# Performance work log

Hardware: AMD Instinct MI355X
Metric: run time of the kernel (lower is better)

## Reference

```python
import jax, jax.numpy as jnp
import numpy as np

S, F, C = 256, 128, 16          # seq_len, n_files, len_feature_columns
T_HEADS, M_HEADS = 5, 4


def _pos_encoding(max_len, d):
    pos = jnp.arange(max_len, dtype=jnp.float32)[:, None]
    div = jnp.exp(jnp.arange(0, d, 2, dtype=jnp.float32) * (-np.log(10000.0) / d))
    pe = jnp.zeros((max_len, d), jnp.float32)
    pe = pe.at[:, 0::2].set(jnp.sin(pos * div))
    pe = pe.at[:, 1::2].set(jnp.cos(pos * div))
    return pe


def _ln(x, w, b, eps=1e-5):
    mu = jnp.mean(x, -1, keepdims=True)
    var = jnp.mean((x - mu) ** 2, -1, keepdims=True)
    return (x - mu) * jax.lax.rsqrt(var + eps) * w + b


def _softmax_kernel(data, proj, is_query, eps=1e-4):
    # FAVOR+ positive softmax random features (lucidrains performer default)
    dh = data.shape[-1]
    m = proj.shape[0]
    dn = dh ** -0.25
    ratio = m ** -0.5
    dd = jnp.einsum('bhnd,md->bhnm', data * dn, proj)
    diag = jnp.sum(data ** 2, -1, keepdims=True) * 0.5 * dn * dn
    stab = jnp.max(dd, -1, keepdims=True) if is_query else jnp.max(dd)
    return ratio * (jnp.exp(dd - diag - stab) + eps)


def _favor_attn(x, wq, wk, wv, wo, wo_b, proj, heads):
    b, n, _ = x.shape
    inner = wq.shape[1]
    dh = inner // heads
    split = lambda t: t.reshape(b, n, heads, dh).transpose(0, 2, 1, 3)
    q, k, v = split(x @ wq), split(x @ wk), split(x @ wv)
    qp = _softmax_kernel(q, proj, True)   # [b,h,n,m]
    kp = _softmax_kernel(k, proj, False)  # [b,h,n,m]
    d_inv = 1.0 / jnp.einsum('bhnm,bhm->bhn', qp, jnp.sum(kp, 2))
    ctx = jnp.einsum('bhnm,bhnd->bhmd', kp, v)            # O(n*m*d) linear attention
    out = jnp.einsum('bhnm,bhmd,bhn->bhnd', qp, ctx, d_inv)
    return out.transpose(0, 2, 1, 3).reshape(b, n, inner) @ wo + wo_b


def _performer(x, p, heads):
    (ln1w, ln1b, wq, wk, wv, wo, wob, ln2w, ln2b, f1w, f1b, f2w, f2b, proj) = p
    for l in range(ln1w.shape[0]):  # depth=4, structurally distinct params
        x = x + _favor_attn(_ln(x, ln1w[l], ln1b[l]), wq[l], wk[l], wv[l], wo[l], wob[l], proj[l], heads)
        h = _ln(x, ln2w[l], ln2b[l])
        x = x + (jax.nn.gelu(h @ f1w[l] + f1b[l]) @ f2w[l] + f2b[l])
    return x


def setup_inputs() -> dict:
    key = jax.random.key(0)
    keys = iter(jax.random.split(key, 80))
    nrm = lambda shape, s=0.02: jax.random.normal(next(keys), shape, jnp.float32) * s
    B = 64
    d = {"x": jax.random.normal(next(keys), (B, S, F * C), jnp.float32),
         "lin_w": nrm((F, C)), "lin_b": jnp.zeros((F,), jnp.float32)}

    def perf(prefix, D, heads, dh, M, L=4):
        I = heads * dh
        d[prefix + "ln1_w"] = jnp.ones((L, D), jnp.float32)
        d[prefix + "ln1_b"] = jnp.zeros((L, D), jnp.float32)
        d[prefix + "wq"] = nrm((L, D, I))
        d[prefix + "wk"] = nrm((L, D, I))
        d[prefix + "wv"] = nrm((L, D, I))
        d[prefix + "wo"] = nrm((L, I, D))
        d[prefix + "wo_b"] = jnp.zeros((L, D), jnp.float32)
        d[prefix + "ln2_w"] = jnp.ones((L, D), jnp.float32)
        d[prefix + "ln2_b"] = jnp.zeros((L, D), jnp.float32)
        d[prefix + "ff1_w"] = nrm((L, D, 4 * D))
        d[prefix + "ff1_b"] = jnp.zeros((L, 4 * D), jnp.float32)
        d[prefix + "ff2_w"] = nrm((L, 4 * D, D))
        d[prefix + "ff2_b"] = jnp.zeros((L, D), jnp.float32)
        d[prefix + "proj"] = jax.random.normal(next(keys), (L, M, dh), jnp.float32)

    perf("t_", S, T_HEADS, S // 2, 620)   # nb_features = int(128*ln 128)
    perf("m_", F, M_HEADS, F // 2, 266)   # nb_features = int(64*ln 64)
    return d


def reference(x, lin_w, lin_b,
              t_ln1_w, t_ln1_b, t_wq, t_wk, t_wv, t_wo, t_wo_b, t_ln2_w, t_ln2_b, t_ff1_w, t_ff1_b, t_ff2_w, t_ff2_b, t_proj,
              m_ln1_w, m_ln1_b, m_wq, m_wk, m_wv, m_wo, m_wo_b, m_ln2_w, m_ln2_b, m_ff1_w, m_ff1_b, m_ff2_w, m_ff2_b, m_proj):
    B = x.shape[0]
    # per-file Linear(C -> 1), concatenated along files: [B,S,F]
    xs = x[:, :S, :].reshape(B, S, F, C)
    lo = jnp.einsum('bsfc,fc->bsf', xs, lin_w) + lin_b
    out = lo.transpose(0, 2, 1)                     # [B,F,S] ticker-major
    out = out + _pos_encoding(F, S)[None]
    tp = (t_ln1_w, t_ln1_b, t_wq, t_wk, t_wv, t_wo, t_wo_b, t_ln2_w, t_ln2_b, t_ff1_w, t_ff1_b, t_ff2_w, t_ff2_b, t_proj)
    out = _performer(out, tp, T_HEADS)
    out = out.transpose(0, 2, 1)                    # [B,S,F] time-major
    out = out + _pos_encoding(S, F)[None]
    mp = (m_ln1_w, m_ln1_b, m_wq, m_wk, m_wv, m_wo, m_wo_b, m_ln2_w, m_ln2_b, m_ff1_w, m_ff1_b, m_ff2_w, m_ff2_b, m_proj)
    out = _performer(out, mp, M_HEADS)
    return out.mean(1)                              # [B,F]
```

## Files before the change

### kernel.cpp

```cpp
#include <hip/hip_runtime.h>
#include <math.h>

using bf16x8 = __attribute__((ext_vector_type(8))) short;
using f32x4  = __attribute__((ext_vector_type(4))) float;
using u16x8  = __attribute__((ext_vector_type(8))) unsigned short;

__device__ __forceinline__ float b2f(unsigned short u){
  union{float f; unsigned int i;} x; x.i = ((unsigned int)u)<<16; return x.f;
}
__device__ __forceinline__ unsigned short f2b(float f){
  union{float f; unsigned int i;} x; x.f = f;
  unsigned int r = x.i + 0x7fffu + ((x.i>>16)&1u);
  return (unsigned short)(r>>16);
}
__device__ __forceinline__ float gelu_tanh(float x){
  float x3 = x*x*x;
  return 0.5f*x*(1.0f + tanhf(0.79788456080286535588f*(x + 0.044715f*x3)));
}
__device__ __forceinline__ float wave_sum(float v){
  #pragma unroll
  for (int o=32;o>0;o>>=1) v += __shfl_down(v,o);
  return v;
}
__device__ __forceinline__ float wave_max(float v){
  #pragma unroll
  for (int o=32;o>0;o>>=1) v = fmaxf(v, __shfl_down(v,o));
  return v;
}
__device__ __forceinline__ unsigned encmax(float f){
  union{float f; unsigned u;} x; x.f = f;
  return (x.u & 0x80000000u) ? ~x.u : (x.u | 0x80000000u);
}
__device__ __forceinline__ float decmax(unsigned e){
  union{unsigned u; float f;} x;
  x.u = (e & 0x80000000u) ? (e & 0x7fffffffu) : ~e;
  return x.f;
}

__global__ __launch_bounds__(256) void k_embed(const float* __restrict__ x,
    const float* __restrict__ lw, const float* __restrict__ lb,
    float* __restrict__ X)
{
  int idx = blockIdx.x*256 + threadIdx.x;
  int s = idx & 255;
  int f = (idx >> 8) & 127;
  int b = idx >> 15;
  const float* xr = x + ((long)(b*256 + s))*2048 + f*16;
  const float* wr = lw + f*16;
  float acc = lb[f];
  #pragma unroll
  for (int c=0;c<16;c++) acc = fmaf(xr[c], wr[c], acc);
  int i = s >> 1;
  float dv = expf((float)(2*i) * (-9.210340371976184f/256.0f));
  float ang = (float)f * dv;
  acc += (s & 1) ? cosf(ang) : sinf(ang);
  X[idx] = acc;
}

__global__ __launch_bounds__(256) void k_transpose_pe(const float* __restrict__ X,
    float* __restrict__ Y)
{
  int idx = blockIdx.x*256 + threadIdx.x;
  int f = idx & 127;
  int s = (idx >> 7) & 255;
  int b = idx >> 15;
  int i = f >> 1;
  float dv = expf((float)(2*i) * (-9.210340371976184f/128.0f));
  float ang = (float)s * dv;
  float pe = (f & 1) ? cosf(ang) : sinf(ang);
  Y[idx] = X[((long)(b*128 + f))*256 + s] + pe;
}

__global__ __launch_bounds__(256) void k_ln(const float* __restrict__ X,
    const float* __restrict__ w, const float* __restrict__ b,
    unsigned short* __restrict__ Y, int R, int D)
{
  int row = blockIdx.x*4 + (threadIdx.x >> 6);
  int lane = threadIdx.x & 63;
  if (row >= R) return;
  const float* xr = X + (long)row*D;
  float sum=0.f, sq=0.f;
  for (int i=lane;i<D;i+=64){ float v=xr[i]; sum+=v; sq+=v*v; }
  sum = wave_sum(sum); sq = wave_sum(sq);
  sum = __shfl(sum,0); sq = __shfl(sq,0);
  float mu = sum/(float)D;
  float var = sq/(float)D - mu*mu;
  float inv = rsqrtf(var + 1e-5f);
  unsigned short* yr = Y + (long)row*D;
  for (int i=lane;i<D;i+=64) yr[i] = f2b((xr[i]-mu)*inv*w[i] + b[i]);
}

struct WTJobs {
  const float* src[12];
  unsigned short* dst[12];
  int K[12]; int N[12];
  long lstr[12];
};
__global__ __launch_bounds__(256) void k_wtall(WTJobs jt)
{
  __shared__ float t[32][33];
  int j = blockIdx.y;
  int K = jt.K[j], N = jt.N[j];
  int nx = N >> 5, ny = K >> 5;
  if ((int)blockIdx.x >= nx*ny) return;
  int nb = ((int)blockIdx.x % nx)*32, kb = ((int)blockIdx.x / nx)*32;
  int l = blockIdx.z;
  const float* Wp = jt.src[j] + (long)l*K*N;
  unsigned short* Tp = jt.dst[j] + (long)l*jt.lstr[j];
  int tx = threadIdx.x & 31, ty = threadIdx.x >> 5;
  #pragma unroll
  for (int i=0;i<4;i++) t[ty+i*8][tx] = Wp[(long)(kb+ty+i*8)*N + nb+tx];
  __syncthreads();
  #pragma unroll
  for (int i=0;i<4;i++) Tp[(long)(nb+ty+i*8)*K + kb+tx] = f2b(t[tx][ty+i*8]);
}

__global__ __launch_bounds__(256) void k_projconv(const float* __restrict__ proj,
    unsigned short* __restrict__ pb, int M, int Mp, int dh, long total)
{
  long idx = (long)blockIdx.x*256 + threadIdx.x;
  if (idx >= total) return;
  int c = (int)(idx % dh);
  long t = idx / dh;
  int m = (int)(t % Mp);
  int l = (int)(t / Mp);
  pb[idx] = (m < M) ? f2b(proj[((long)l*M + m)*dh + c]) : (unsigned short)0;
}

template<bool A_CM, bool B_CM, int EPI, bool OUT_BF16, bool EXPB, int MAXM, bool KSUM,
         int DIAGM, int TM>
__global__ __launch_bounds__(256) void k_mgemm(
    const void* __restrict__ A, const void* __restrict__ B, void* __restrict__ C,
    const float* __restrict__ bias, const float* __restrict__ res,
    const float* __restrict__ ediag, const unsigned* __restrict__ estab,
    unsigned* __restrict__ maxu, float* __restrict__ ksumio,
    float* __restrict__ diagp, float dnn, int nseq, int diagH,
    float ratio, float eps, int Mvalid,
    float alpha, int H, int R, int NC, int K,
    long Ab, long Ah, long lda,
    long Bb, long Bh, long ldb,
    long Cb, long Ch, long ldc)
{
  constexpr int CF  = (TM==128) ? 4 : 2;
  constexpr int AIT = (TM==128) ? 2 : 1;
  __shared__ unsigned short Asm[TM][40];
  __shared__ unsigned short Bsm[128][40];
  __shared__ float sred[4];
  __shared__ float ks_lds[KSUM?16:1][KSUM?132:1];
  __shared__ float dg2[DIAGM==1?128:1][DIAGM==1?2:1];
  const int tid = threadIdx.x;
  const int bz = blockIdx.z;
  const int b = bz / H, h = bz - b*H;
  const unsigned short* Ap16 = (const unsigned short*)A + (long)b*Ab + (long)h*Ah;
  const unsigned short* Bp16 = (const unsigned short*)B + (long)b*Bb + (long)h*Bh;
  const int r0 = blockIdx.y*TM, c0 = blockIdx.x*128;
  const int wid = tid>>6, lane = tid&63;
  const int wr = wid>>1, wc = wid&1;
  const int lr = lane&15, lg = lane>>4;
  const int WRO = (TM==128) ? wr*64 : 0;
  const int WCO = (TM==128) ? wc*64 : wid*32;
  float stabB = 0.f;
  if (EXPB) stabB = decmax(estab[0]);
  float kpart[KSUM?8:1] = {};
  f32x4 acc[4][CF] = {};

  u16x8 pA[AIT], pB[2];
  float pDg[2];
  auto loadA = [&](int k0){
    if constexpr (!A_CM){
      #pragma unroll
      for (int it=0; it<AIT; ++it){
        int idx = tid + it*256;
        int r = idx>>2, kq = (idx&3)*8;
        pA[it] = *reinterpret_cast<const u16x8*>(Ap16 + (long)(r0+r)*lda + (k0+kq));
      }
    } else {
      #pragma unroll
      for (int it=0; it<AIT; ++it){
        int idx = tid + it*256;
        int k = idx>>4, rq = (idx&15)*8;
        u16x8 v = {};
        if (r0+rq < R) v = *reinterpret_cast<const u16x8*>(Ap16 + (long)(k0+k)*lda + (r0+rq));
        pA[it] = v;
      }
    }
  };
  auto writeA = [&](){
    if constexpr (!A_CM){
      #pragma unroll
      for (int it=0; it<AIT; ++it){
        int idx = tid + it*256;
        int r = idx>>2, kq = (idx&3)*8;
        *reinterpret_cast<u16x8*>(&Asm[r][kq]) = pA[it];
      }
    } else {
      #pragma unroll
      for (int it=0; it<AIT; ++it){
        int idx = tid + it*256;
        int k = idx>>4, rq = (idx&15)*8;
        #pragma unroll
        for (int i=0;i<8;i++){
          int rr = rq + i;
          int sc = (k&7) | ((((k>>3) ^ ((rr>>3)&3)))<<3);
          Asm[rr][sc] = pA[it][i];
        }
      }
    }
  };
  auto loadB = [&](int k0){
    if constexpr (EXPB){
      #pragma unroll
      for (int it=0; it<2; ++it){
        int idx = tid + it*256;
        int k = idx>>4, cq = (idx&15)*8;
        pDg[it] = ediag[(long)bz*K + (k0+k)];
        u16x8 v = {};
        if (c0+cq < NC) v = *reinterpret_cast<const u16x8*>(Bp16 + (long)(k0+k)*ldb + (c0+cq));
        pB[it] = v;
      }
    } else if constexpr (B_CM){
      #pragma unroll
      for (int it=0; it<2; ++it){
        int idx = tid + it*256;
        int c = idx>>2, kq = (idx&3)*8;
        u16x8 v = {};
        if (c0+c < NC) v = *reinterpret_cast<const u16x8*>(Bp16 + (long)(c0+c)*ldb + (k0+kq));
        pB[it] = v;
      }
    } else {
      #pragma unroll
      for (int it=0; it<2; ++it){
        int idx = tid + it*256;
        int k = idx>>4, cq = (idx&15)*8;
        u16x8 v = {};
        if (c0+cq < NC) v = *reinterpret_cast<const u16x8*>(Bp16 + (long)(k0+k)*ldb + (c0+cq));
        pB[it] = v;
      }
    }
  };
  auto writeB = [&](int k0){
    if constexpr (EXPB){
      #pragma unroll
      for (int it=0; it<2; ++it){
        int idx = tid + it*256;
        int k = idx>>4, cq = (idx&15)*8;
        bool inb = (c0+cq < NC);
        #pragma unroll
        for (int i=0;i<8;i++){
          int c = c0+cq+i;
          float v = (c < Mvalid && inb) ? ratio*(expf(b2f(pB[it][i])-pDg[it]-stabB)+eps) : 0.0f;
          int rr = cq + i;
          int sc = (k&7) | ((((k>>3) ^ ((rr>>3)&3)))<<3);
          Bsm[rr][sc] = f2b(v);
          if (KSUM) kpart[i] += v;
        }
      }
    } else if constexpr (B_CM){
      #pragma unroll
      for (int it=0; it<2; ++it){
        int idx = tid + it*256;
        int c = idx>>2, kq = (idx&3)*8;
        *reinterpret_cast<u16x8*>(&Bsm[c][kq]) = pB[it];
      }
    } else {
      #pragma unroll
      for (int it=0; it<2; ++it){
        int idx = tid + it*256;
        int k = idx>>4, cq = (idx&15)*8;
        #pragma unroll
        for (int i=0;i<8;i++) Bsm[cq+i][k] = pB[it][i];
      }
    }
  };

  loadA(0); loadB(0);
  for (int k0=0; k0<K; k0+=32){
    writeA(); writeB(k0);
    __syncthreads();
    if (k0+32 < K){ loadA(k0+32); loadB(k0+32); }
    bf16x8 af[4], bfr[CF];
    #pragma unroll
    for (int m=0;m<4;m++){
      int arow = WRO + m*16 + lr;
      int acol8 = A_CM ? (lg ^ ((arow>>3)&3)) : lg;
      af[m] = *reinterpret_cast<const bf16x8*>(&Asm[arow][acol8*8]);
    }
    #pragma unroll
    for (int n=0;n<CF;n++){
      int brow = WCO + n*16 + lr;
      int bcol8 = EXPB ? (lg ^ ((brow>>3)&3)) : lg;
      bfr[n] = *reinterpret_cast<const bf16x8*>(&Bsm[brow][bcol8*8]);
    }
    #pragma unroll
    for (int m=0;m<4;m++)
      #pragma unroll
      for (int n=0;n<CF;n++)
        acc[m][n] = __builtin_amdgcn_mfma_f32_16x16x32_bf16(af[m], bfr[n], acc[m][n], 0, 0, 0);
    __syncthreads();
  }

  if constexpr (MAXM==1){
    float mx = -INFINITY;
    #pragma unroll
    for (int m=0;m<4;m++)
      #pragma unroll
      for (int n=0;n<CF;n++)
        #pragma unroll
        for (int e=0;e<4;e++) mx = fmaxf(mx, acc[m][n][e]);
    mx *= alpha;
    mx = wave_max(mx);
    if (lane==0) sred[wid]=mx;
    __syncthreads();
    if (tid==0) atomicMax(maxu, encmax(fmaxf(fmaxf(sred[0],sred[1]),fmaxf(sred[2],sred[3]))));
  }
  if constexpr (KSUM){
    #pragma unroll
    for (int j=0;j<8;j++) ks_lds[tid>>4][(tid&15)*8+j] = kpart[j];
    __syncthreads();
    if (tid < 128){
      float s = 0.f;
      #pragma unroll
      for (int g=0;g<16;g++) s += ks_lds[g][tid];
      int gc = c0 + tid;
      if (gc < NC) ksumio[(long)bz*NC + gc] = s;
    }
  }

  float* Cf = (float*)C;
  unsigned short* Cb16 = (unsigned short*)C;
  const long coff = (long)b*Cb + (long)h*Ch;
  #pragma unroll
  for (int m=0;m<4;m++){
    #pragma unroll
    for (int n=0;n<CF;n++){
      #pragma unroll
      for (int e=0;e<4;e++){
        int r = WRO + m*16 + lg*4 + e;
        int c = WCO + n*16 + lr;
        int gr = r0 + r, gc = c0 + c;
        if (gr < R && gc < NC){
          float v = acc[m][n][e] * alpha;
          if (EPI >= 2) v += bias[gc];
          if (EPI == 2) v = gelu_tanh(v);
          if (EPI == 3) v += res[(long)gr*ldc + gc];
          long o = coff + (long)gr*ldc + gc;
          if (OUT_BF16) Cb16[o] = f2b(v); else Cf[o] = v;
        }
      }
    }
  }

  if constexpr (DIAGM>0){
    if (bz == 0 && blockIdx.x == 0 && blockIdx.y == 0 && tid == 0) maxu[0] = 0u;
    if (bz < 2){
      const long soff = (long)bz * (long)R * diagH;
      #pragma unroll
      for (int m=0;m<4;m++)
        #pragma unroll
        for (int e=0;e<4;e++){
          int r = WRO + m*16 + lg*4 + e;
          float s = 0.f;
          #pragma unroll
          for (int nn=0;nn<CF;nn++) s = fmaf(acc[m][nn][e], acc[m][nn][e], s);
          #pragma unroll
          for (int o=1;o<16;o<<=1) s += __shfl_xor(s, o);
          if (lr==0){
            if constexpr (DIAGM==2){
              int gr = r0 + r;
              int bb = gr / nseq, ni = gr - bb*nseq;
              int hh = (int)blockIdx.x*2 + wc;
              diagp[soff + ((long)bb*diagH + hh)*nseq + ni] = dnn*s;
            } else {
              dg2[r][wc] = s;
            }
          }
        }
      if constexpr (DIAGM==1){
        __syncthreads();
        if (tid < 128){
          int gr = r0 + tid;
          int bb = gr / nseq, ni = gr - bb*nseq;
          int hh = (int)blockIdx.x;
          diagp[soff + ((long)bb*diagH + hh)*nseq + ni] = dnn*(dg2[tid][0] + dg2[tid][1]);
        }
      }
    }
  }
}

template<int DH, int MP, int MM, int NCH, int NOUT>
__global__ __launch_bounds__(512) void k_qout(
    const unsigned short* __restrict__ Qb,
    const unsigned short* __restrict__ proj,
    const unsigned short* __restrict__ CTXT,
    const float* __restrict__ diagq,
    const float* __restrict__ ksum,
    unsigned short* __restrict__ out,
    float dn, float ratio, float eps,
    int H, int n, int I)
{
  constexpr int QP = DH + 8;
  constexpr int BSZ = (64*QP > DH*72) ? 64*QP : DH*72;
  constexpr int NST = DH/32;
  constexpr int NQS = (64*(DH/8) + 511)/512;
  constexpr int NCS = (DH*8 + 511)/512;
  __shared__ unsigned short Qs[64][QP];
  __shared__ unsigned short qp[64][72];
  __shared__ unsigned short Bs[BSZ];
  __shared__ float ks_all[MP];
  __shared__ float diag_lds[64], rmax4[4][64], qs4[4][64], dinv_lds[64];
  const int tid = threadIdx.x;
  const int bz = blockIdx.x;
  const int b = bz / H, h = bz - b*H;
  const int ni0 = blockIdx.y*64;
  const int wid = tid>>6, lane = tid&63;
  const int wr = wid>>2, wc = wid&3;
  const int lr = lane&15, lg = lane>>4;
  const long ctxoff = (long)bz*DH*MP;

  u16x8 rP[NQS], rC[NCS];
  auto ldP = [&](int mc){
    #pragma unroll
    for (int it=0; it<NQS; ++it){
      int idx = tid + it*512;
      int c = idx/(DH/8), seg = idx%(DH/8);
      int mg = mc*64 + c;
      rP[it] = (mg < MP) ? *reinterpret_cast<const u16x8*>(proj + (long)mg*DH + seg*8) : u16x8{};
    }
  };
  auto stP = [&](){
    #pragma unroll
    for (int it=0; it<NQS; ++it){
      int idx = tid + it*512;
      int c = idx/(DH/8), seg = idx%(DH/8);
      *reinterpret_cast<u16x8*>(&Bs[c*QP + seg*8]) = rP[it];
    }
  };
  auto ldC = [&](int mc){
    #pragma unroll
    for (int it=0; it<NCS; ++it){
      int idx = tid + it*512;
      int c = idx>>3, kseg = idx&7;
      int kg = mc*64 + kseg*8;
      rC[it] = (kg < MP) ? *reinterpret_cast<const u16x8*>(CTXT + ctxoff + (long)c*MP + kg) : u16x8{};
    }
  };
  auto stC = [&](){
    #pragma unroll
    for (int it=0; it<NCS; ++it){
      int idx = tid + it*512;
      int c = idx>>3, kseg = idx&7;
      *reinterpret_cast<u16x8*>(&Bs[c*72 + kseg*8]) = rC[it];
    }
  };

  const unsigned short* Qp = Qb + ((long)(b*n + ni0))*I + h*DH;
  #pragma unroll
  for (int it=0; it<NQS; ++it){
    int idx = tid + it*512;
    int r = idx/(DH/8), seg = idx%(DH/8);
    *reinterpret_cast<u16x8*>(&Qs[r][seg*8]) =
        *reinterpret_cast<const u16x8*>(Qp + (long)r*I + seg*8);
  }
  for (int i=tid;i<MP;i+=512) ks_all[i] = ksum[(long)bz*MP + i];
  if (tid < 64) diag_lds[tid] = diagq[(long)bz*n + ni0 + tid];
  ldP(0);
  stP();
  __syncthreads();

  float rmax[2][4];
  #pragma unroll
  for (int m=0;m<2;m++)
    #pragma unroll
    for (int e=0;e<4;e++) rmax[m][e] = -INFINITY;
  for (int mc=0; mc<NCH; ++mc){
    if (mc+1 < NCH) ldP(mc+1);
    f32x4 dacc[2] = {};
    __builtin_amdgcn_s_setprio(1);
    #pragma unroll
    for (int ks=0; ks<NST; ++ks){
      bf16x8 bf_ = *reinterpret_cast<const bf16x8*>(&Bs[(wc*16+lr)*QP + ks*32 + lg*8]);
      #pragma unroll
      for (int m=0;m<2;m++){
        bf16x8 af = *reinterpret_cast<const bf16x8*>(&Qs[wr*32+m*16+lr][ks*32+lg*8]);
        dacc[m] = __builtin_amdgcn_mfma_f32_16x16x32_bf16(af, bf_, dacc[m], 0, 0, 0);
      }
    }
    __builtin_amdgcn_s_setprio(0);
    {
      int col = mc*64 + wc*16 + lr;
      if (col < MM){
        #pragma unroll
        for (int m=0;m<2;m++)
          #pragma unroll
          for (int e=0;e<4;e++) rmax[m][e] = fmaxf(rmax[m][e], dacc[m][e]*dn);
      }
    }
    __syncthreads();
    if (mc+1 < NCH){ stP(); __syncthreads(); }
  }
  #pragma unroll
  for (int m=0;m<2;m++)
    #pragma unroll
    for (int e=0;e<4;e++){
      #pragma unroll
      for (int o=1;o<16;o<<=1) rmax[m][e] = fmaxf(rmax[m][e], __shfl_xor(rmax[m][e], o));
      if (lr==0) rmax4[wc][wr*32+m*16+lg*4+e] = rmax[m][e];
    }
  __syncthreads();
  if (tid < 64)
    rmax4[0][tid] = fmaxf(fmaxf(rmax4[0][tid], rmax4[1][tid]),
                          fmaxf(rmax4[2][tid], rmax4[3][tid]));
  ldP(0);
  __syncthreads();
  stP();
  __syncthreads();

  float qsum[2][4] = {};
  f32x4 oacc[2][NOUT] = {};
  for (int mc=0; mc<NCH; ++mc){
    ldC(mc);
    f32x4 dacc[2] = {};
    __builtin_amdgcn_s_setprio(1);
    #pragma unroll
    for (int ks=0; ks<NST; ++ks){
      bf16x8 bf_ = *reinterpret_cast<const bf16x8*>(&Bs[(wc*16+lr)*QP + ks*32 + lg*8]);
      #pragma unroll
      for (int m=0;m<2;m++){
        bf16x8 af = *reinterpret_cast<const bf16x8*>(&Qs[wr*32+m*16+lr][ks*32+lg*8]);
        dacc[m] = __builtin_amdgcn_mfma_f32_16x16x32_bf16(af, bf_, dacc[m], 0, 0, 0);
      }
    }
    __builtin_amdgcn_s_setprio(0);
    __syncthreads();
    stC();
    {
      int lc = wc*16 + lr;
      int col = mc*64 + lc;
      bool valid = (col < MM);
      float kv = valid ? ks_all[col] : 0.f;
      #pragma unroll
      for (int m=0;m<2;m++)
        #pragma unroll
        for (int e=0;e<4;e++){
          int row = wr*32+m*16+lg*4+e;
          float v = 0.f;
          if (valid){
            v = ratio*(expf(dacc[m][e]*dn - diag_lds[row] - rmax4[0][row]) + eps);
            qsum[m][e] = fmaf(v, kv, qsum[m][e]);
          }
          qp[row][lc] = f2b(v);
        }
    }
    __syncthreads();
    if (mc+1 < NCH) ldP(mc+1);
    __builtin_amdgcn_s_setprio(1);
    #pragma unroll
    for (int ks=0; ks<2; ++ks){
      bf16x8 af[2];
      #pragma unroll
      for (int m=0;m<2;m++) af[m] = *reinterpret_cast<const bf16x8*>(&qp[wr*32+m*16+lr][ks*32+lg*8]);
      #pragma unroll
      for (int nn=0;nn<NOUT;nn++){
        bf16x8 bf_ = *reinterpret_cast<const bf16x8*>(&Bs[(wc*(DH/4)+nn*16+lr)*72 + ks*32 + lg*8]);
        #pragma unroll
        for (int m=0;m<2;m++)
          oacc[m][nn] = __builtin_amdgcn_mfma_f32_16x16x32_bf16(af[m], bf_, oacc[m][nn], 0, 0, 0);
      }
    }
    __builtin_amdgcn_s_setprio(0);
    __syncthreads();
    if (mc+1 < NCH){ stP(); __syncthreads(); }
  }

  #pragma unroll
  for (int m=0;m<2;m++)
    #pragma unroll
    for (int e=0;e<4;e++){
      float s = qsum[m][e];
      #pragma unroll
      for (int o=1;o<16;o<<=1) s += __shfl_xor(s, o);
      if (lr==0) qs4[wc][wr*32+m*16+lg*4+e] = s;
    }
  __syncthreads();
  if (tid < 64) dinv_lds[tid] = 1.0f/(qs4[0][tid] + qs4[1][tid] + qs4[2][tid] + qs4[3][tid]);
  __syncthreads();

  unsigned short* Op = out + ((long)(b*n + ni0))*I + h*DH;
  #pragma unroll
  for (int m=0;m<2;m++)
    #pragma unroll
    for (int e=0;e<4;e++){
      int row = wr*32+m*16+lg*4+e;
      float di = dinv_lds[row];
      #pragma unroll
      for (int nn=0;nn<NOUT;nn++){
        int c = wc*(DH/4)+nn*16+lr;
        Op[(long)row*I + c] = f2b(oacc[m][nn][e]*di);
      }
    }
}

__global__ __launch_bounds__(256) void k_mean(const float* __restrict__ X,
    float* __restrict__ out)
{
  int idx = blockIdx.x*256 + threadIdx.x;
  int f = idx & 127, b = idx >> 7;
  const float* p = X + (long)b*256*128 + f;
  float s = 0.f;
  for (int i=0;i<256;i++) s += p[i*128];
  out[idx] = s*(1.0f/256.0f);
}

struct StageP {
  const float *ln1w,*ln1b,*wob,*ln2w,*ln2b,*f1b,*f2b;
  const unsigned short *wkqvT,*woT,*f1T,*f2T,*projb;
  int n, D, H, dh, I, M, Mp;
};

template<int DH, int MP, int MM, int NCH, int NOUT, int DGM>
static void run_stage(const StageP& P, float* X, unsigned short* LNb,
    unsigned short* KQVb, unsigned short* DDk, unsigned short* CTXT,
    unsigned short* ATTNb, unsigned short* FFHb,
    float* KPSUM, float* DIAG, unsigned* REDU,
    hipStream_t stream)
{
  const int B = 64;
  const int rows = B*P.n;
  const int bh = B*P.H;
  const int bhn = bh*P.n;
  const float dn = powf((float)P.dh, -0.25f);
  const float dnn = 0.5f*dn*dn;
  const float ratio = 1.0f/sqrtf((float)P.M);
  const float eps = 1e-4f;

  const unsigned short* Kb = KQVb;
  const unsigned short* Qb = KQVb + (long)rows*P.I;
  const unsigned short* Vb = KQVb + 2L*rows*P.I;
  const float* DIAGK = DIAG;
  const float* DIAGQ = DIAG + bhn;

  for (int l=0;l<4;l++){
    const float* ln1w = P.ln1w + (long)l*P.D;
    const float* ln1b = P.ln1b + (long)l*P.D;
    const float* wob  = P.wob  + (long)l*P.D;
    const float* ln2w = P.ln2w + (long)l*P.D;
    const float* ln2b = P.ln2b + (long)l*P.D;
    const float* f1b  = P.f1b  + (long)l*4*P.D;
    const float* f2b_ = P.f2b  + (long)l*P.D;
    const unsigned short* wkqvT = P.wkqvT + (long)l*3*P.D*P.I;
    const unsigned short* woT = P.woT + (long)l*P.I*P.D;
    const unsigned short* f1T = P.f1T + (long)l*P.D*4*P.D;
    const unsigned short* f2T = P.f2T + (long)l*4*P.D*P.D;
    const unsigned short* pjb = P.projb + (long)l*P.Mp*P.dh;

    k_ln<<<dim3((rows+3)/4),dim3(256),0,stream>>>(X, ln1w, ln1b, LNb, rows, P.D);
    dim3 gq(P.I/128, rows/128, 3);
    k_mgemm<false,true,0,true,false,0,false,DGM,128><<<gq,dim3(256),0,stream>>>(
        LNb, wkqvT, KQVb, nullptr,nullptr, nullptr,nullptr, REDU, nullptr,
        DIAG, dnn, P.n, P.H,
        0,0,0, 1.f, 1, rows, P.I, P.D,
        0,0,(long)P.D,
        (long)P.I*P.D,0,(long)P.D,
        (long)rows*P.I,0,(long)P.I);
    dim3 gdd((P.Mp+127)/128, P.n/128, bh);
    k_mgemm<false,true,0,true,false,1,false,0,128><<<gdd,dim3(256),0,stream>>>(
        Kb, pjb, DDk, nullptr,nullptr, nullptr,nullptr, REDU, nullptr,
        nullptr, 0.f, 0, 0,
        0,0,0, dn, P.H, P.n, P.Mp, P.dh,
        (long)P.n*P.I, (long)P.dh, (long)P.I,
        0, 0, (long)P.dh,
        (long)P.H*P.n*P.Mp, (long)P.n*P.Mp, (long)P.Mp);
    dim3 gctx((P.Mp+127)/128, (P.dh+127)/128, bh);
    k_mgemm<true,false,0,true,true,0,true,0,128><<<gctx,dim3(256),0,stream>>>(
        Vb, DDk, CTXT, nullptr,nullptr, DIAGK, REDU, nullptr, KPSUM,
        nullptr, 0.f, 0, 0,
        ratio, eps, P.M,
        1.f, P.H, P.dh, P.Mp, P.n,
        (long)P.n*P.I, (long)P.dh, (long)P.I,
        (long)P.H*P.n*P.Mp, (long)P.n*P.Mp, (long)P.Mp,
        (long)P.H*P.dh*P.Mp, (long)P.dh*P.Mp, (long)P.Mp);
    dim3 gqo(bh, P.n/64, 1);
    k_qout<DH,MP,MM,NCH,NOUT><<<gqo,dim3(512),0,stream>>>(
        Qb, pjb, CTXT, DIAGQ, KPSUM, ATTNb, dn, ratio, eps, P.H, P.n, P.I);
    dim3 gwo(P.D/128, rows/64, 1);
    k_mgemm<false,true,3,false,false,0,false,0,64><<<gwo,dim3(256),0,stream>>>(
        ATTNb, woT, X, wob, X, nullptr,nullptr, nullptr,nullptr,
        nullptr, 0.f, 0, 0,
        0,0,0, 1.f, 1, rows, P.D, P.I, 0,0,(long)P.I, 0,0,(long)P.I, 0,0,(long)P.D);
    k_ln<<<dim3((rows+3)/4),dim3(256),0,stream>>>(X, ln2w, ln2b, LNb, rows, P.D);
    dim3 gf1(4*P.D/128, rows/128, 1);
    k_mgemm<false,true,2,true,false,0,false,0,128><<<gf1,dim3(256),0,stream>>>(
        LNb, f1T, FFHb, f1b, nullptr, nullptr,nullptr, nullptr,nullptr,
        nullptr, 0.f, 0, 0,
        0,0,0, 1.f, 1, rows, 4*P.D, P.D, 0,0,(long)P.D, 0,0,(long)P.D, 0,0,(long)(4*P.D));
    dim3 gf2(P.D/128, rows/64, 1);
    k_mgemm<false,true,3,false,false,0,false,0,64><<<gf2,dim3(256),0,stream>>>(
        FFHb, f2T, X, f2b_, X, nullptr,nullptr, nullptr,nullptr,
        nullptr, 0.f, 0, 0,
        0,0,0, 1.f, 1, rows, P.D, 4*P.D, 0,0,(long)(4*P.D), 0,0,(long)(4*P.D), 0,0,(long)P.D);
  }
}

extern "C" void kernel_launch(void* const* d_in, const int* in_sizes, int n_in,
                              void* d_out, int out_size, void* d_ws, size_t ws_size,
                              hipStream_t stream)
{
  const float* x     = (const float*)d_in[0];
  const float* lin_w = (const float*)d_in[1];
  const float* lin_b = (const float*)d_in[2];

  char* wsb = (char*)d_ws;
  size_t off = 0;
  auto alloc = [&](size_t bytes)->void*{ void* p = wsb + off; off += (bytes + 255) & ~(size_t)255; return p; };
  float* X     = (float*)alloc(8388608);
  float* X2    = (float*)alloc(8388608);
  unsigned short* LNb   = (unsigned short*)alloc(4194304);
  unsigned short* KQVb  = (unsigned short*)alloc(31457280);
  unsigned short* DDk   = (unsigned short*)alloc(52428800);
  unsigned short* CTXT  = (unsigned short*)alloc(52428800);
  unsigned short* ATTNb = (unsigned short*)alloc(10485760);
  unsigned short* WKQV1 = (unsigned short*)alloc(3932160);
  unsigned short* WO1T  = (unsigned short*)alloc(1310720);
  unsigned short* F11T  = (unsigned short*)alloc(2097152);
  unsigned short* F21T  = (unsigned short*)alloc(2097152);
  unsigned short* WKQV2 = (unsigned short*)alloc(786432);
  unsigned short* WO2T  = (unsigned short*)alloc(262144);
  unsigned short* F12T  = (unsigned short*)alloc(524288);
  unsigned short* F22T  = (unsigned short*)alloc(524288);
  unsigned short* PJ1   = (unsigned short*)alloc(655360);
  unsigned short* PJ2   = (unsigned short*)alloc(147456);
  float* KPSUM = (float*)alloc(819200);
  float* DIAG  = (float*)alloc(524288);
  unsigned* REDU = (unsigned*)alloc(256);
  unsigned short* FFHb = DDk;
  if (ws_size < off) return;

  WTJobs jt;
  jt.src[0]=(const float*)d_in[6];  jt.dst[0]=WKQV1+0L*640*256;  jt.K[0]=256; jt.N[0]=640;  jt.lstr[0]=3L*640*256;
  jt.src[1]=(const float*)d_in[5];  jt.dst[1]=WKQV1+1L*640*256;  jt.K[1]=256; jt.N[1]=640;  jt.lstr[1]=3L*640*256;
  jt.src[2]=(const float*)d_in[7];  jt.dst[2]=WKQV1+2L*640*256;  jt.K[2]=256; jt.N[2]=640;  jt.lstr[2]=3L*640*256;
  jt.src[3]=(const float*)d_in[8];  jt.dst[3]=WO1T;              jt.K[3]=640; jt.N[3]=256;  jt.lstr[3]=640L*256;
  jt.src[4]=(const float*)d_in[12]; jt.dst[4]=F11T;              jt.K[4]=256; jt.N[4]=1024; jt.lstr[4]=1024L*256;
  jt.src[5]=(const float*)d_in[14]; jt.dst[5]=F21T;              jt.K[5]=1024;jt.N[5]=256;  jt.lstr[5]=1024L*256;
  jt.src[6]=(const float*)d_in[20]; jt.dst[6]=WKQV2+0L*256*128;  jt.K[6]=128; jt.N[6]=256;  jt.lstr[6]=3L*256*128;
  jt.src[7]=(const float*)d_in[19]; jt.dst[7]=WKQV2+1L*256*128;  jt.K[7]=128; jt.N[7]=256;  jt.lstr[7]=3L*256*128;
  jt.src[8]=(const float*)d_in[21]; jt.dst[8]=WKQV2+2L*256*128;  jt.K[8]=128; jt.N[8]=256;  jt.lstr[8]=3L*256*128;
  jt.src[9]=(const float*)d_in[22]; jt.dst[9]=WO2T;              jt.K[9]=256; jt.N[9]=128;  jt.lstr[9]=256L*128;
  jt.src[10]=(const float*)d_in[26];jt.dst[10]=F12T;             jt.K[10]=128;jt.N[10]=512; jt.lstr[10]=512L*128;
  jt.src[11]=(const float*)d_in[28];jt.dst[11]=F22T;             jt.K[11]=512;jt.N[11]=128; jt.lstr[11]=512L*128;
  k_wtall<<<dim3(256,12,4),dim3(256),0,stream>>>(jt);
  {
    long t1 = 4L*640*128;
    k_projconv<<<dim3((int)((t1+255)/256)),dim3(256),0,stream>>>((const float*)d_in[16], PJ1, 620, 640, 128, t1);
    long t2 = 4L*288*64;
    k_projconv<<<dim3((int)((t2+255)/256)),dim3(256),0,stream>>>((const float*)d_in[30], PJ2, 266, 288, 64, t2);
  }

  StageP T;
  T.ln1w=(const float*)d_in[3];  T.ln1b=(const float*)d_in[4];
  T.wob=(const float*)d_in[9];
  T.ln2w=(const float*)d_in[10]; T.ln2b=(const float*)d_in[11];
  T.f1b=(const float*)d_in[13];  T.f2b=(const float*)d_in[15];
  T.wkqvT=WKQV1; T.woT=WO1T; T.f1T=F11T; T.f2T=F21T; T.projb=PJ1;
  T.n=128; T.D=256; T.H=5; T.dh=128; T.I=640; T.M=620; T.Mp=640;

  StageP Ms;
  Ms.ln1w=(const float*)d_in[17]; Ms.ln1b=(const float*)d_in[18];
  Ms.wob=(const float*)d_in[23];
  Ms.ln2w=(const float*)d_in[24]; Ms.ln2b=(const float*)d_in[25];
  Ms.f1b=(const float*)d_in[27];  Ms.f2b=(const float*)d_in[29];
  Ms.wkqvT=WKQV2; Ms.woT=WO2T; Ms.f1T=F12T; Ms.f2T=F22T; Ms.projb=PJ2;
  Ms.n=256; Ms.D=128; Ms.H=4; Ms.dh=64; Ms.I=256; Ms.M=266; Ms.Mp=288;

  k_embed<<<dim3(8192),dim3(256),0,stream>>>(x, lin_w, lin_b, X);
  run_stage<128,640,620,10,2,1>(T, X, LNb, KQVb, DDk, CTXT, ATTNb, FFHb,
            KPSUM, DIAG, REDU, stream);
  k_transpose_pe<<<dim3(8192),dim3(256),0,stream>>>(X, X2);
  run_stage<64,288,266,5,1,2>(Ms, X2, LNb, KQVb, DDk, CTXT, ATTNb, FFHb,
            KPSUM, DIAG, REDU, stream);
  k_mean<<<dim3(32),dim3(256),0,stream>>>(X2, (float*)d_out);
}
```

Baseline: 1.879 ms.

## Keep Q fragments in registers and split P/C LDS buffers to drop barriers

The kernel now loads the Q A-operand fragments straight from global memory into registers, replacing the shared Qs tile. The shared Bs buffer, which held both the projection tile and the context tile, becomes two separate buffers (Pb, Cb). Because the two tiles no longer alias, the output loop can write the context tile and the next projection tile without waiting at an extra barrier first, which removes two __syncthreads per chunk. In exchange, register pressure rises (2*NST bf16x8 fragments held across both loops) and total LDS use grows, which may lower occupancy.

After: 1.824 ms. 2.9% less time.

```diff
diff --git a/kernel.cpp b/kernel.cpp
--- a/kernel.cpp
+++ b/kernel.cpp
@@ -400,13 +400,12 @@
     int H, int n, int I)
 {
   constexpr int QP = DH + 8;
-  constexpr int BSZ = (64*QP > DH*72) ? 64*QP : DH*72;
   constexpr int NST = DH/32;
   constexpr int NQS = (64*(DH/8) + 511)/512;
   constexpr int NCS = (DH*8 + 511)/512;
-  __shared__ unsigned short Qs[64][QP];
+  __shared__ unsigned short Pb[64][QP];
+  __shared__ unsigned short Cb[DH][72];
   __shared__ unsigned short qp[64][72];
-  __shared__ unsigned short Bs[BSZ];
   __shared__ float ks_all[MP];
   __shared__ float diag_lds[64], rmax4[4][64], qs4[4][64], dinv_lds[64];
   const int tid = threadIdx.x;
@@ -433,7 +432,7 @@
     for (int it=0; it<NQS; ++it){
       int idx = tid + it*512;
       int c = idx/(DH/8), seg = idx%(DH/8);
-      *reinterpret_cast<u16x8*>(&Bs[c*QP + seg*8]) = rP[it];
+      *reinterpret_cast<u16x8*>(&Pb[c][seg*8]) = rP[it];
     }
   };
   auto ldC = [&](int mc){
@@ -450,17 +449,18 @@
     for (int it=0; it<NCS; ++it){
       int idx = tid + it*512;
       int c = idx>>3, kseg = idx&7;
-      *reinterpret_cast<u16x8*>(&Bs[c*72 + kseg*8]) = rC[it];
+      *reinterpret_cast<u16x8*>(&Cb[c][kseg*8]) = rC[it];
     }
   };
 
   const unsigned short* Qp = Qb + ((long)(b*n + ni0))*I + h*DH;
-  #pragma unroll
-  for (int it=0; it<NQS; ++it){
-    int idx = tid + it*512;
-    int r = idx/(DH/8), seg = idx%(DH/8);
-    *reinterpret_cast<u16x8*>(&Qs[r][seg*8]) =
-        *reinterpret_cast<const u16x8*>(Qp + (long)r*I + seg*8);
+  bf16x8 aq[2][NST];
+  #pragma unroll
+  for (int m=0;m<2;m++){
+    int qrow = wr*32 + m*16 + lr;
+    #pragma unroll
+    for (int ks=0;ks<NST;ks++)
+      aq[m][ks] = *reinterpret_cast<const bf16x8*>(Qp + (long)qrow*I + ks*32 + lg*8);
   }
   for (int i=tid;i<MP;i+=512) ks_all[i] = ksum[(long)bz*MP + i];
   if (tid < 64) diag_lds[tid] = diagq[(long)bz*n + ni0 + tid];
@@ -479,12 +479,10 @@
     __builtin_amdgcn_s_setprio(1);
     #pragma unroll
     for (int ks=0; ks<NST; ++ks){
-      bf16x8 bf_ = *reinterpret_cast<const bf16x8*>(&Bs[(wc*16+lr)*QP + ks*32 + lg*8]);
-      #pragma unroll
-      for (int m=0;m<2;m++){
-        bf16x8 af = *reinterpret_cast<const bf16x8*>(&Qs[wr*32+m*16+lr][ks*32+lg*8]);
-        dacc[m] = __builtin_amdgcn_mfma_f32_16x16x32_bf16(af, bf_, dacc[m], 0, 0, 0);
-      }
+      bf16x8 bf_ = *reinterpret_cast<const bf16x8*>(&Pb[wc*16+lr][ks*32 + lg*8]);
+      #pragma unroll
+      for (int m=0;m<2;m++)
+        dacc[m] = __builtin_amdgcn_mfma_f32_16x16x32_bf16(aq[m][ks], bf_, dacc[m], 0, 0, 0);
     }
     __builtin_amdgcn_s_setprio(0);
     {
@@ -524,16 +522,12 @@
     __builtin_amdgcn_s_setprio(1);
     #pragma unroll
     for (int ks=0; ks<NST; ++ks){
-      bf16x8 bf_ = *reinterpret_cast<const bf16x8*>(&Bs[(wc*16+lr)*QP + ks*32 + lg*8]);
-      #pragma unroll
-      for (int m=0;m<2;m++){
-        bf16x8 af = *reinterpret_cast<const bf16x8*>(&Qs[wr*32+m*16+lr][ks*32+lg*8]);
-        dacc[m] = __builtin_amdgcn_mfma_f32_16x16x32_bf16(af, bf_, dacc[m], 0, 0, 0);
-      }
+      bf16x8 bf_ = *reinterpret_cast<const bf16x8*>(&Pb[wc*16+lr][ks*32 + lg*8]);
+      #pragma unroll
+      for (int m=0;m<2;m++)
+        dacc[m] = __builtin_amdgcn_mfma_f32_16x16x32_bf16(aq[m][ks], bf_, dacc[m], 0, 0, 0);
     }
     __builtin_amdgcn_s_setprio(0);
-    __syncthreads();
-    stC();
     {
       int lc = wc*16 + lr;
       int col = mc*64 + lc;
@@ -552,8 +546,9 @@
           qp[row][lc] = f2b(v);
         }
     }
+    stC();
+    if (mc+1 < NCH) ldP(mc+1);
     __syncthreads();
-    if (mc+1 < NCH) ldP(mc+1);
     __builtin_amdgcn_s_setprio(1);
     #pragma unroll
     for (int ks=0; ks<2; ++ks){
@@ -562,15 +557,15 @@
       for (int m=0;m<2;m++) af[m] = *reinterpret_cast<const bf16x8*>(&qp[wr*32+m*16+lr][ks*32+lg*8]);
       #pragma unroll
       for (int nn=0;nn<NOUT;nn++){
-        bf16x8 bf_ = *reinterpret_cast<const bf16x8*>(&Bs[(wc*(DH/4)+nn*16+lr)*72 + ks*32 + lg*8]);
+        bf16x8 bf_ = *reinterpret_cast<const bf16x8*>(&Cb[wc*(DH/4)+nn*16+lr][ks*32 + lg*8]);
         #pragma unroll
         for (int m=0;m<2;m++)
           oacc[m][nn] = __builtin_amdgcn_mfma_f32_16x16x32_bf16(af[m], bf_, oacc[m][nn], 0, 0, 0);
       }
     }
     __builtin_amdgcn_s_setprio(0);
+    if (mc+1 < NCH) stP();
     __syncthreads();
-    if (mc+1 < NCH){ stP(); __syncthreads(); }
   }
 
   #pragma unroll
```
